# Kernel optimization log

Hardware: AMD Instinct MI355X
Metric: run time of the kernel (lower is better)

## Reference

```python
import jax, jax.numpy as jnp
import numpy as np

N_NODES = 100000
N_EDGES = 1600000
IN_DIM, HID_DIM, OUT_DIM = 128, 64, 1


def setup_inputs() -> dict:
    key = jax.random.key(0)
    ks = jax.random.split(key, 8)
    x = jax.random.normal(ks[0], (N_NODES, IN_DIM), dtype=jnp.float32)
    edge_index = jax.random.randint(ks[1], (2, N_EDGES), 0, N_NODES, dtype=jnp.int64)
    # Glorot-ish scaled weights
    W1 = jax.random.normal(ks[2], (IN_DIM, HID_DIM), dtype=jnp.float32) / np.sqrt(IN_DIM)
    b1 = jnp.zeros((HID_DIM,), dtype=jnp.float32)
    W2 = jax.random.normal(ks[3], (HID_DIM, HID_DIM), dtype=jnp.float32) / np.sqrt(HID_DIM)
    b2 = jnp.zeros((HID_DIM,), dtype=jnp.float32)
    W3 = jax.random.normal(ks[4], (HID_DIM, OUT_DIM), dtype=jnp.float32) / np.sqrt(HID_DIM)
    b3 = jnp.zeros((OUT_DIM,), dtype=jnp.float32)
    return {"x": x, "edge_index": edge_index, "W1": W1, "b1": b1,
            "W2": W2, "b2": b2, "W3": W3, "b3": b3}


def _gcn_norm(edge_index, num_nodes):
    # PyG gcn_norm with add_self_loops=True, edge_weight=1:
    # deg[i] = 1 (self loop) + #incoming edges at i (dst = edge_index[1])
    dst = edge_index[1]
    deg = jnp.ones((num_nodes,), dtype=jnp.float32).at[dst].add(1.0)
    dis = jnp.where(deg > 0, 1.0 / jnp.sqrt(deg), 0.0)  # deg_inv_sqrt
    return dis


def _gcn_conv(x, W, b, src, dst, dis):
    h = x @ W                                   # [N, F_out] transform first (PyG order)
    norm = dis[src] * dis[dst]                  # [E]
    msg = h[src] * norm[:, None]                # gather + scale, [E, F_out]
    out = jnp.zeros_like(h).at[dst].add(msg)    # scatter-add aggregation
    out = out + h * (dis * dis)[:, None]        # self-loop contribution
    return out + b


def reference(x, edge_index, W1, b1, W2, b2, W3, b3):
    src, dst = edge_index[0], edge_index[1]
    dis = _gcn_norm(edge_index, x.shape[0])
    h = jax.nn.relu(_gcn_conv(x, W1, b1, src, dst, dis))   # dropout = identity (eval)
    h = jax.nn.relu(_gcn_conv(h, W2, b2, src, dst, dis))
    return _gcn_conv(h, W3, b3, src, dst, dis)
```

## Files before the change

kernel.cpp:

```cpp
#include <hip/hip_runtime.h>

#define IN_DIM 128
#define HID 64
#define MAXC 400
#define MAXB 256
#define EPB 8192
#define DPT 1024
#define G1CAP 6144

static __device__ __forceinline__ unsigned short f2bf(float f) {
    unsigned u = __float_as_uint(f);
    u += 0x7FFF + ((u >> 16) & 1);
    return (unsigned short)(u >> 16);
}

typedef short bf16x8 __attribute__((ext_vector_type(8)));
typedef float f32x4 __attribute__((ext_vector_type(4)));

__global__ __launch_bounds__(256) void k_hist2(const int* __restrict__ dst,
                                               int* __restrict__ hmat, int E, int NC) {
    __shared__ int h[MAXC];
    int tid = threadIdx.x, blk = blockIdx.x;
    for (int i = tid; i < NC; i += 256) h[i] = 0;
    __syncthreads();
    int e0 = blk * EPB, e1 = min(e0 + EPB, E);
    for (int e = e0 + tid; e < e1; e += 256) atomicAdd(&h[dst[e] >> 8], 1);
    __syncthreads();
    for (int i = tid; i < NC; i += 256) hmat[blk * MAXC + i] = h[i];
}

__global__ __launch_bounds__(256) void k_bktscan(int* __restrict__ hmat,
                                                 int* __restrict__ bktTotal,
                                                 int NBLK, int NC) {
    __shared__ int tmp[256];
    int cb = blockIdx.x;
    int t = threadIdx.x;
    int v = (t < NBLK) ? hmat[t * MAXC + cb] : 0;
    tmp[t] = v;
    __syncthreads();
    for (int off = 1; off < 256; off <<= 1) {
        int a = (t >= off) ? tmp[t - off] : 0;
        __syncthreads();
        tmp[t] += a;
        __syncthreads();
    }
    if (t < NBLK) hmat[t * MAXC + cb] = tmp[t] - v;
    if (t == 255) bktTotal[cb] = tmp[255];
}

__global__ __launch_bounds__(512) void k_cscan(const int* __restrict__ bktTotal,
                                               int* __restrict__ coarseStart,
                                               int* __restrict__ rowStart,
                                               int NC, int N, int E) {
    __shared__ int tmp[512];
    int t = threadIdx.x;
    int v = (t < NC) ? bktTotal[t] : 0;
    tmp[t] = v;
    __syncthreads();
    for (int off = 1; off < 512; off <<= 1) {
        int a = (t >= off) ? tmp[t - off] : 0;
        __syncthreads();
        tmp[t] += a;
        __syncthreads();
    }
    int excl = tmp[t] - v;
    if (t < NC) coarseStart[t] = excl;
    if (t == NC - 1) coarseStart[NC] = excl + v;
    if (t == 0) rowStart[N] = E;
}

__global__ __launch_bounds__(256) void k_part1(const int* __restrict__ src,
                                               const int* __restrict__ dst,
                                               const int* __restrict__ hmat,
                                               const int* __restrict__ coarseStart,
                                               int* __restrict__ tmp1,
                                               int E, int NC) {
    __shared__ int bcnt[MAXC];
    __shared__ int bbase[MAXC];
    int tid = threadIdx.x, blk = blockIdx.x;
    for (int i = tid; i < NC; i += 256) {
        bcnt[i] = 0;
        bbase[i] = coarseStart[i] + hmat[blk * MAXC + i];
    }
    __syncthreads();
    int e0 = blk * EPB, e1 = min(e0 + EPB, E);
    for (int e = e0 + tid; e < e1; e += 256) {
        int s = src[e], d = dst[e];
        int cb = d >> 8;
        int slot = bbase[cb] + atomicAdd(&bcnt[cb], 1);
        tmp1[slot] = s | ((d & 255) << 17);
    }
}

__global__ __launch_bounds__(DPT) void k_degplace(const int* __restrict__ tmp1,
                                                  const int* __restrict__ coarseStart,
                                                  float* __restrict__ dis,
                                                  int* __restrict__ rowStart,
                                                  int* __restrict__ esrc, int N) {
    __shared__ int hist[256];
    __shared__ int scn[256];
    __shared__ int cur[256];
    int tid = threadIdx.x;
    int cb = blockIdx.x;
    int node0 = cb << 8;
    const int r0 = coarseStart[cb], r1 = coarseStart[cb + 1];
    if (tid < 256) hist[tid] = 0;
    __syncthreads();
    for (int i = r0 + tid; i < r1; i += DPT)
        atomicAdd(&hist[((unsigned)tmp1[i]) >> 17], 1);
    __syncthreads();
    int v = 0;
    if (tid < 256) { v = hist[tid]; scn[tid] = v; }
    __syncthreads();
    for (int off = 1; off < 256; off <<= 1) {
        int a = 0;
        if (tid < 256 && tid >= off) a = scn[tid - off];
        __syncthreads();
        if (tid < 256) scn[tid] += a;
        __syncthreads();
    }
    if (tid < 256) {
        int myStart = r0 + scn[tid] - v;
        cur[tid] = myStart;
        int node = node0 + tid;
        if (node < N) {
            dis[node] = rsqrtf((float)v + 1.0f);
            rowStart[node] = myStart;
        }
    }
    __syncthreads();
    for (int i = r0 + tid; i < r1; i += DPT) {
        int pk = tmp1[i];
        int dl = ((unsigned)pk) >> 17;
        int pos = atomicAdd(&cur[dl], 1);
        esrc[pos] = (pk & 0x1FFFF) << 7;
    }
}

template <int K, typename T>
__global__ __launch_bounds__(256) void k_mmx(const T* __restrict__ X,
                                             const float* __restrict__ W,
                                             const float* __restrict__ dis,
                                             unsigned short* __restrict__ Hbs, int N) {
    constexpr int WP = K + 8;
    __shared__ unsigned short Wt[64 * WP];
    const int tid = threadIdx.x;
    for (int i = tid; i < K * 64; i += 256) {
        int k = i >> 6, n = i & 63;
        Wt[n * WP + k] = f2bf(W[i]);
    }
    __syncthreads();
    const int lane = tid & 63;
    const int m16 = lane & 15;
    const int quad = lane >> 4;
    const int rowBase = blockIdx.x * 64 + (tid >> 6) * 16;
    const int rowc = min(rowBase + m16, N - 1);

    f32x4 acc0 = {0.f, 0.f, 0.f, 0.f};
    f32x4 acc1 = acc0, acc2 = acc0, acc3 = acc0;
    const T* xrow = X + (size_t)rowc * K;
#pragma unroll
    for (int k0 = 0; k0 < K; k0 += 32) {
        bf16x8 af;
        if constexpr (sizeof(T) == 4) {
            const float* xp = (const float*)xrow + k0 + quad * 8;
            float4 xa = *(const float4*)xp;
            float4 xb = *(const float4*)(xp + 4);
            af[0] = (short)f2bf(xa.x); af[1] = (short)f2bf(xa.y);
            af[2] = (short)f2bf(xa.z); af[3] = (short)f2bf(xa.w);
            af[4] = (short)f2bf(xb.x); af[5] = (short)f2bf(xb.y);
            af[6] = (short)f2bf(xb.z); af[7] = (short)f2bf(xb.w);
        } else {
            af = *(const bf16x8*)((const unsigned short*)xrow + k0 + quad * 8);
        }
        const unsigned short* wp = &Wt[m16 * WP + k0 + quad * 8];
        bf16x8 b0 = *(const bf16x8*)(wp);
        bf16x8 b1 = *(const bf16x8*)(wp + 16 * WP);
        bf16x8 b2 = *(const bf16x8*)(wp + 32 * WP);
        bf16x8 b3 = *(const bf16x8*)(wp + 48 * WP);
        acc0 = __builtin_amdgcn_mfma_f32_16x16x32_bf16(af, b0, acc0, 0, 0, 0);
        acc1 = __builtin_amdgcn_mfma_f32_16x16x32_bf16(af, b1, acc1, 0, 0, 0);
        acc2 = __builtin_amdgcn_mfma_f32_16x16x32_bf16(af, b2, acc2, 0, 0, 0);
        acc3 = __builtin_amdgcn_mfma_f32_16x16x32_bf16(af, b3, acc3, 0, 0, 0);
    }
#pragma unroll
    for (int reg = 0; reg < 4; ++reg) {
        int r = rowBase + quad * 4 + reg;
        if (r < N) {
            float dsc = dis[r];
            unsigned short* hp = Hbs + (size_t)r * 64 + m16;
            hp[0]  = f2bf(acc0[reg] * dsc);
            hp[16] = f2bf(acc1[reg] * dsc);
            hp[32] = f2bf(acc2[reg] * dsc);
            hp[48] = f2bf(acc3[reg] * dsc);
        }
    }
}


#define ACCADD(A, D)                                                           \
    {                                                                          \
        A.x += __uint_as_float((D).x << 16);                                   \
        A.y += __uint_as_float((D).x & 0xFFFF0000u);                           \
        A.z += __uint_as_float((D).y << 16);                                   \
        A.w += __uint_as_float((D).y & 0xFFFF0000u);                           \
    }

#define GNODE4(ACC, RA, RB)                                                    \
    {                                                                          \
        int j0 = max(RA - base, 0);                                            \
        int j1 = min(RB - base, cnt);                                          \
        int j = j0;                                                            \
        for (; j + 16 <= j1; j += 16) {                                        \
            unsigned o0 = __shfl(eoff, j + sub, 64);                           \
            unsigned o1 = __shfl(eoff, j + 4 + sub, 64);                       \
            unsigned o2 = __shfl(eoff, j + 8 + sub, 64);                       \
            unsigned o3 = __shfl(eoff, j + 12 + sub, 64);                      \
            uint2 q0 = *(const uint2*)(hb + o0);                               \
            uint2 q1 = *(const uint2*)(hb + o1);                               \
            uint2 q2 = *(const uint2*)(hb + o2);                               \
            uint2 q3 = *(const uint2*)(hb + o3);                               \
            ACCADD(ACC, q0) ACCADD(ACC, q1) ACCADD(ACC, q2) ACCADD(ACC, q3)    \
        }                                                                      \
        if (j + 8 <= j1) {                                                     \
            unsigned o0 = __shfl(eoff, j + sub, 64);                           \
            unsigned o1 = __shfl(eoff, j + 4 + sub, 64);                       \
            uint2 q0 = *(const uint2*)(hb + o0);                               \
            uint2 q1 = *(const uint2*)(hb + o1);                               \
            ACCADD(ACC, q0) ACCADD(ACC, q1)                                    \
            j += 8;                                                            \
        }                                                                      \
        if (j + 4 <= j1) {                                                     \
            unsigned o0 = __shfl(eoff, j + sub, 64);                           \
            uint2 q0 = *(const uint2*)(hb + o0);                               \
            ACCADD(ACC, q0)                                                    \
            j += 4;                                                            \
        }                                                                      \
        if (j < j1) {                                                          \
            int idx = j + sub;                                                 \
            bool vld = idx < j1;                                               \
            unsigned o0 = __shfl(eoff, vld ? idx : j0, 64);                    \
            uint2 q0 = *(const uint2*)(hb + o0);                               \
            if (!vld) { q0.x = 0u; q0.y = 0u; }                                \
            ACCADD(ACC, q0)                                                    \
        }                                                                      \
    }

#define REDX(A)                                                                \
    {                                                                          \
        A.x += __shfl_xor(A.x, 16, 64); A.y += __shfl_xor(A.y, 16, 64);        \
        A.z += __shfl_xor(A.z, 16, 64); A.w += __shfl_xor(A.w, 16, 64);        \
        A.x += __shfl_xor(A.x, 32, 64); A.y += __shfl_xor(A.y, 32, 64);        \
        A.z += __shfl_xor(A.z, 32, 64); A.w += __shfl_xor(A.w, 32, 64);        \
    }

template <int MODE>
__global__ __launch_bounds__(256) void k_gather64(const unsigned short* __restrict__ Hbs,
                                                  const int* __restrict__ esrc,
                                                  const int* __restrict__ rowStart,
                                                  const float* __restrict__ dis,
                                                  const float* __restrict__ b,
                                                  unsigned short* __restrict__ outB,
                                                  const float* __restrict__ W3,
                                                  const float* __restrict__ b3,
                                                  float* __restrict__ colS,
                                                  float* __restrict__ outF,
                                                  int N) {
    int lane = threadIdx.x & 63;
    int c = lane & 15;
    int sub = lane >> 4;
    int wave = (blockIdx.x * 256 + threadIdx.x) >> 6;
    int g0 = wave * 4;
    if (g0 >= N) return;
    const char* hb = (const char*)Hbs + c * 8;

    int rb = rowStart[min(g0 + lane, N)];
    int R0 = __shfl(rb, 0, 64), R1 = __shfl(rb, 1, 64);
    int R2 = __shfl(rb, 2, 64), R3 = __shfl(rb, 3, 64);
    int R4 = __shfl(rb, 4, 64);

    float4 a0 = {0.f, 0.f, 0.f, 0.f}, a1 = a0, a2 = a0, a3 = a0;
    {
        int nself = min(g0 + sub, N - 1);
        uint2 sd = *(const uint2*)(hb + ((size_t)nself << 7));
        float4 sf;
        sf.x = __uint_as_float(sd.x << 16);
        sf.y = __uint_as_float(sd.x & 0xFFFF0000u);
        sf.z = __uint_as_float(sd.y << 16);
        sf.w = __uint_as_float(sd.y & 0xFFFF0000u);
        if (sub == 0) a0 = sf;
        else if (sub == 1) a1 = sf;
        else if (sub == 2) a2 = sf;
        else a3 = sf;
    }

    for (int base = R0; base < R4; base += 64) {
        int cnt = min(64, R4 - base);
        unsigned eoff = (lane < cnt) ? (unsigned)esrc[base + lane] : 0u;
        GNODE4(a0, R0, R1)
        GNODE4(a1, R1, R2)
        GNODE4(a2, R2, R3)
        GNODE4(a3, R3, R4)
    }

    REDX(a0) REDX(a1) REDX(a2) REDX(a3)

    float4 a = a0;
    if (sub == 1) a = a1;
    if (sub == 2) a = a2;
    if (sub == 3) a = a3;
    int node = g0 + sub;
    float ds = dis[min(node, N - 1)];
    float4 bl = ((const float4*)b)[c];
    float4 v;
    v.x = fmaxf(a.x * ds + bl.x, 0.f);
    v.y = fmaxf(a.y * ds + bl.y, 0.f);
    v.z = fmaxf(a.z * ds + bl.z, 0.f);
    v.w = fmaxf(a.w * ds + bl.w, 0.f);

    if (MODE == 1) {
        uint2 pv;
        pv.x = (unsigned)f2bf(v.x) | ((unsigned)f2bf(v.y) << 16);
        pv.y = (unsigned)f2bf(v.z) | ((unsigned)f2bf(v.w) << 16);
        if (node < N) ((uint2*)outB)[(size_t)node * 16 + c] = pv;
    } else {
        float4 w3 = ((const float4*)W3)[c];
        float t = v.x * w3.x + v.y * w3.y + v.z * w3.z + v.w * w3.w;
        t += __shfl_xor(t, 1, 64);
        t += __shfl_xor(t, 2, 64);
        t += __shfl_xor(t, 4, 64);
        t += __shfl_xor(t, 8, 64);
        if (c == 0 && node < N) {
            colS[node] = t * ds;
            outF[node] = t * ds * ds + b3[0];
        }
    }
}

__global__ __launch_bounds__(256) void k_gather1(const float* __restrict__ colS,
                                                 const int* __restrict__ esrc,
                                                 const int* __restrict__ rowStart,
                                                 const float* __restrict__ dis,
                                                 float* __restrict__ out, int N) {
    __shared__ float ls[G1CAP];
    int tid = threadIdx.x;
    int n0 = blockIdx.x * 256;
    int nEnd = min(n0 + 256, N);
    int r0 = rowStart[n0];
    int r1 = rowStart[nEnd];
    int cnt = r1 - r0;
    if (cnt <= G1CAP) {
        for (int i = tid; i < cnt; i += 256)
            ls[i] = colS[((unsigned)esrc[r0 + i]) >> 7];
        __syncthreads();
        int n = n0 + tid;
        if (n < N) {
            int a = rowStart[n] - r0, bnd = rowStart[n + 1] - r0;
            float acc = 0.0f;
            for (int e = a; e < bnd; ++e) acc += ls[e];
            out[n] += acc * dis[n];
        }
    } else {
        int n = n0 + tid;
        if (n < N) {
            int a = rowStart[n], bnd = rowStart[n + 1];
            float acc = 0.0f;
            for (int e = a; e < bnd; ++e) acc += colS[((unsigned)esrc[e]) >> 7];
            out[n] += acc * dis[n];
        }
    }
}

extern "C" void kernel_launch(void* const* d_in, const int* in_sizes, int n_in,
                              void* d_out, int out_size, void* d_ws, size_t ws_size,
                              hipStream_t stream) {
    const float* x  = (const float*)d_in[0];
    const int*   ei = (const int*)d_in[1];
    const float* W1 = (const float*)d_in[2];
    const float* b1 = (const float*)d_in[3];
    const float* W2 = (const float*)d_in[4];
    const float* b2 = (const float*)d_in[5];
    const float* W3 = (const float*)d_in[6];
    const float* b3 = (const float*)d_in[7];
    float* out = (float*)d_out;

    const int N = in_sizes[0] / IN_DIM;
    const int E = in_sizes[1] / 2;
    const int* src = ei;
    const int* dst = ei + E;
    const int NC = (N + 255) >> 8;
    const int NBLK = (E + EPB - 1) / EPB;

    char* w = (char*)d_ws;
    auto alloc = [&](size_t bytes) {
        char* p = w;
        w += (bytes + 1023) & ~(size_t)1023;
        return p;
    };
    float*          dis        = (float*)alloc((size_t)N * 4);
    unsigned short* Hbs        = (unsigned short*)alloc((size_t)N * 64 * 2);
    unsigned short* Hb1        = (unsigned short*)alloc((size_t)N * 64 * 2);
    float*          colS       = (float*)alloc((size_t)N * 4);
    int*            rowStart   = (int*)alloc((size_t)(N + 1) * 4);
    int*            bktTotal   = (int*)alloc((size_t)MAXC * 4);
    int*            coarseStart= (int*)alloc((size_t)(MAXC + 1) * 4);
    int*            hmat       = (int*)alloc((size_t)MAXB * MAXC * 4);
    int*            esrc       = (int*)alloc((size_t)E * 4);
    int*            tmp1       = (int*)alloc((size_t)E * 4);

    const int NB_N  = (N + 255) / 256;
    const int NB_MX = (N + 63) / 64;
    const int NB_G4 = ((N + 3) / 4 * 64 + 255) / 256;

    k_hist2<<<NBLK, 256, 0, stream>>>(dst, hmat, E, NC);
    k_bktscan<<<NC, 256, 0, stream>>>(hmat, bktTotal, NBLK, NC);
    k_cscan<<<1, 512, 0, stream>>>(bktTotal, coarseStart, rowStart, NC, N, E);
    k_part1<<<NBLK, 256, 0, stream>>>(src, dst, hmat, coarseStart, tmp1, E, NC);
    k_degplace<<<NC, DPT, 0, stream>>>(tmp1, coarseStart, dis, rowStart, esrc, N);

    k_mmx<IN_DIM, float><<<NB_MX, 256, 0, stream>>>(x, W1, dis, Hbs, N);
    k_gather64<1><<<NB_G4, 256, 0, stream>>>(Hbs, esrc, rowStart, dis, b1,
                                             Hb1, nullptr, nullptr, nullptr, nullptr, N);

    k_mmx<HID, unsigned short><<<NB_MX, 256, 0, stream>>>(Hb1, W2, dis, Hbs, N);
    k_gather64<2><<<NB_G4, 256, 0, stream>>>(Hbs, esrc, rowStart, dis, b2,
                                             nullptr, W3, b3, colS, out, N);

    k_gather1<<<NB_N, 256, 0, stream>>>(colS, esrc, rowStart, dis, out, N);
}
```

Baseline: 242.3 us.

## Assign one node per quarter-wave in GCN gather and retune CSR build sizes

```diff
diff --git a/kernel.cpp b/kernel.cpp
--- a/kernel.cpp
+++ b/kernel.cpp
@@ -3,9 +3,9 @@
 #define IN_DIM 128
 #define HID 64
 #define MAXC 400
-#define MAXB 256
-#define EPB 8192
-#define DPT 1024
+#define MAXB 512
+#define EPB 4096
+#define DPT 512
 #define G1CAP 6144
 
 static __device__ __forceinline__ unsigned short f2bf(float f) {
@@ -29,23 +29,23 @@
     for (int i = tid; i < NC; i += 256) hmat[blk * MAXC + i] = h[i];
 }
 
-__global__ __launch_bounds__(256) void k_bktscan(int* __restrict__ hmat,
+__global__ __launch_bounds__(512) void k_bktscan(int* __restrict__ hmat,
                                                  int* __restrict__ bktTotal,
                                                  int NBLK, int NC) {
-    __shared__ int tmp[256];
+    __shared__ int tmp[512];
     int cb = blockIdx.x;
     int t = threadIdx.x;
     int v = (t < NBLK) ? hmat[t * MAXC + cb] : 0;
     tmp[t] = v;
     __syncthreads();
-    for (int off = 1; off < 256; off <<= 1) {
+    for (int off = 1; off < 512; off <<= 1) {
         int a = (t >= off) ? tmp[t - off] : 0;
         __syncthreads();
         tmp[t] += a;
         __syncthreads();
     }
     if (t < NBLK) hmat[t * MAXC + cb] = tmp[t] - v;
-    if (t == 255) bktTotal[cb] = tmp[255];
+    if (t == 511) bktTotal[cb] = tmp[511];
 }
 
 __global__ __launch_bounds__(512) void k_cscan(const int* __restrict__ bktTotal,
@@ -198,61 +198,10 @@
 }
 
 
-#define ACCADD(A, D)                                                           \
-    {                                                                          \
-        A.x += __uint_as_float((D).x << 16);                                   \
-        A.y += __uint_as_float((D).x & 0xFFFF0000u);                           \
-        A.z += __uint_as_float((D).y << 16);                                   \
-        A.w += __uint_as_float((D).y & 0xFFFF0000u);                           \
-    }
-
-#define GNODE4(ACC, RA, RB)                                                    \
-    {                                                                          \
-        int j0 = max(RA - base, 0);                                            \
-        int j1 = min(RB - base, cnt);                                          \
-        int j = j0;                                                            \
-        for (; j + 16 <= j1; j += 16) {                                        \
-            unsigned o0 = __shfl(eoff, j + sub, 64);                           \
-            unsigned o1 = __shfl(eoff, j + 4 + sub, 64);                       \
-            unsigned o2 = __shfl(eoff, j + 8 + sub, 64);                       \
-            unsigned o3 = __shfl(eoff, j + 12 + sub, 64);                      \
-            uint2 q0 = *(const uint2*)(hb + o0);                               \
-            uint2 q1 = *(const uint2*)(hb + o1);                               \
-            uint2 q2 = *(const uint2*)(hb + o2);                               \
-            uint2 q3 = *(const uint2*)(hb + o3);                               \
-            ACCADD(ACC, q0) ACCADD(ACC, q1) ACCADD(ACC, q2) ACCADD(ACC, q3)    \
-        }                                                                      \
-        if (j + 8 <= j1) {                                                     \
-            unsigned o0 = __shfl(eoff, j + sub, 64);                           \
-            unsigned o1 = __shfl(eoff, j + 4 + sub, 64);                       \
-            uint2 q0 = *(const uint2*)(hb + o0);                               \
-            uint2 q1 = *(const uint2*)(hb + o1);                               \
-            ACCADD(ACC, q0) ACCADD(ACC, q1)                                    \
-            j += 8;                                                            \
-        }                                                                      \
-        if (j + 4 <= j1) {                                                     \
-            unsigned o0 = __shfl(eoff, j + sub, 64);                           \
-            uint2 q0 = *(const uint2*)(hb + o0);                               \
-            ACCADD(ACC, q0)                                                    \
-            j += 4;                                                            \
-        }                                                                      \
-        if (j < j1) {                                                          \
-            int idx = j + sub;                                                 \
-            bool vld = idx < j1;                                               \
-            unsigned o0 = __shfl(eoff, vld ? idx : j0, 64);                    \
-            uint2 q0 = *(const uint2*)(hb + o0);                               \
-            if (!vld) { q0.x = 0u; q0.y = 0u; }                                \
-            ACCADD(ACC, q0)                                                    \
-        }                                                                      \
-    }
-
-#define REDX(A)                                                                \
-    {                                                                          \
-        A.x += __shfl_xor(A.x, 16, 64); A.y += __shfl_xor(A.y, 16, 64);        \
-        A.z += __shfl_xor(A.z, 16, 64); A.w += __shfl_xor(A.w, 16, 64);        \
-        A.x += __shfl_xor(A.x, 32, 64); A.y += __shfl_xor(A.y, 32, 64);        \
-        A.z += __shfl_xor(A.z, 32, 64); A.w += __shfl_xor(A.w, 32, 64);        \
-    }
+#define BLO(d) __uint_as_float((d) << 16)
+#define BHI(d) __uint_as_float((d) & 0xFFFF0000u)
+#define ACC2(A, Q) { A.x += BLO((Q).x); A.y += BHI((Q).x);                     \
+                     A.z += BLO((Q).y); A.w += BHI((Q).y); }
 
 template <int MODE>
 __global__ __launch_bounds__(256) void k_gather64(const unsigned short* __restrict__ Hbs,
@@ -269,48 +218,78 @@
     int lane = threadIdx.x & 63;
     int c = lane & 15;
     int sub = lane >> 4;
+    int qb = sub << 4;
     int wave = (blockIdx.x * 256 + threadIdx.x) >> 6;
     int g0 = wave * 4;
     if (g0 >= N) return;
     const char* hb = (const char*)Hbs + c * 8;
 
     int rb = rowStart[min(g0 + lane, N)];
-    int R0 = __shfl(rb, 0, 64), R1 = __shfl(rb, 1, 64);
-    int R2 = __shfl(rb, 2, 64), R3 = __shfl(rb, 3, 64);
-    int R4 = __shfl(rb, 4, 64);
-
-    float4 a0 = {0.f, 0.f, 0.f, 0.f}, a1 = a0, a2 = a0, a3 = a0;
+    int Rq  = __shfl(rb, sub, 64);
+    int Rq1 = __shfl(rb, sub + 1, 64);
+    int n = g0 + sub;
+    int nc = min(n, N - 1);
+
+    float4 a;
     {
-        int nself = min(g0 + sub, N - 1);
-        uint2 sd = *(const uint2*)(hb + ((size_t)nself << 7));
-        float4 sf;
-        sf.x = __uint_as_float(sd.x << 16);
-        sf.y = __uint_as_float(sd.x & 0xFFFF0000u);
-        sf.z = __uint_as_float(sd.y << 16);
-        sf.w = __uint_as_float(sd.y & 0xFFFF0000u);
-        if (sub == 0) a0 = sf;
-        else if (sub == 1) a1 = sf;
-        else if (sub == 2) a2 = sf;
-        else a3 = sf;
-    }
-
-    for (int base = R0; base < R4; base += 64) {
-        int cnt = min(64, R4 - base);
-        unsigned eoff = (lane < cnt) ? (unsigned)esrc[base + lane] : 0u;
-        GNODE4(a0, R0, R1)
-        GNODE4(a1, R1, R2)
-        GNODE4(a2, R2, R3)
-        GNODE4(a3, R3, R4)
-    }
-
-    REDX(a0) REDX(a1) REDX(a2) REDX(a3)
-
-    float4 a = a0;
-    if (sub == 1) a = a1;
-    if (sub == 2) a = a2;
-    if (sub == 3) a = a3;
-    int node = g0 + sub;
-    float ds = dis[min(node, N - 1)];
+        uint2 sd = *(const uint2*)(hb + ((size_t)nc << 7));
+        a.x = BLO(sd.x); a.y = BHI(sd.x); a.z = BLO(sd.y); a.w = BHI(sd.y);
+    }
+
+    unsigned eoff = (Rq + c < Rq1) ? (unsigned)esrc[Rq + c] : 0u;
+    for (int bb = Rq; bb < Rq1; bb += 16) {
+        int cnt = min(16, Rq1 - bb);
+        unsigned eoffN = (bb + 16 + c < Rq1) ? (unsigned)esrc[bb + 16 + c] : 0u;
+
+        int j = 0;
+        for (; j + 8 <= cnt; j += 8) {
+            unsigned o0 = __shfl(eoff, qb + j + 0, 64);
+            unsigned o1 = __shfl(eoff, qb + j + 1, 64);
+            unsigned o2 = __shfl(eoff, qb + j + 2, 64);
+            unsigned o3 = __shfl(eoff, qb + j + 3, 64);
+            unsigned o4 = __shfl(eoff, qb + j + 4, 64);
+            unsigned o5 = __shfl(eoff, qb + j + 5, 64);
+            unsigned o6 = __shfl(eoff, qb + j + 6, 64);
+            unsigned o7 = __shfl(eoff, qb + j + 7, 64);
+            uint2 q0 = *(const uint2*)(hb + o0);
+            uint2 q1 = *(const uint2*)(hb + o1);
+            uint2 q2 = *(const uint2*)(hb + o2);
+            uint2 q3 = *(const uint2*)(hb + o3);
+            uint2 q4 = *(const uint2*)(hb + o4);
+            uint2 q5 = *(const uint2*)(hb + o5);
+            uint2 q6 = *(const uint2*)(hb + o6);
+            uint2 q7 = *(const uint2*)(hb + o7);
+            ACC2(a, q0) ACC2(a, q1) ACC2(a, q2) ACC2(a, q3)
+            ACC2(a, q4) ACC2(a, q5) ACC2(a, q6) ACC2(a, q7)
+        }
+        if (j + 4 <= cnt) {
+            unsigned o0 = __shfl(eoff, qb + j + 0, 64);
+            unsigned o1 = __shfl(eoff, qb + j + 1, 64);
+            unsigned o2 = __shfl(eoff, qb + j + 2, 64);
+            unsigned o3 = __shfl(eoff, qb + j + 3, 64);
+            uint2 q0 = *(const uint2*)(hb + o0);
+            uint2 q1 = *(const uint2*)(hb + o1);
+            uint2 q2 = *(const uint2*)(hb + o2);
+            uint2 q3 = *(const uint2*)(hb + o3);
+            ACC2(a, q0) ACC2(a, q1) ACC2(a, q2) ACC2(a, q3)
+            j += 4;
+        }
+        if (j < cnt) {
+            bool v1 = j + 1 < cnt, v2 = j + 2 < cnt;
+            unsigned o0 = __shfl(eoff, qb + j, 64);
+            unsigned o1 = __shfl(eoff, v1 ? qb + j + 1 : qb + j, 64);
+            unsigned o2 = __shfl(eoff, v2 ? qb + j + 2 : qb + j, 64);
+            uint2 q0 = *(const uint2*)(hb + o0);
+            uint2 q1 = *(const uint2*)(hb + o1);
+            uint2 q2 = *(const uint2*)(hb + o2);
+            if (!v1) { q1.x = 0u; q1.y = 0u; }
+            if (!v2) { q2.x = 0u; q2.y = 0u; }
+            ACC2(a, q0) ACC2(a, q1) ACC2(a, q2)
+        }
+        eoff = eoffN;
+    }
+
+    float ds = dis[nc];
     float4 bl = ((const float4*)b)[c];
     float4 v;
     v.x = fmaxf(a.x * ds + bl.x, 0.f);
@@ -322,7 +301,7 @@
         uint2 pv;
         pv.x = (unsigned)f2bf(v.x) | ((unsigned)f2bf(v.y) << 16);
         pv.y = (unsigned)f2bf(v.z) | ((unsigned)f2bf(v.w) << 16);
-        if (node < N) ((uint2*)outB)[(size_t)node * 16 + c] = pv;
+        if (n < N) ((uint2*)outB)[(size_t)n * 16 + c] = pv;
     } else {
         float4 w3 = ((const float4*)W3)[c];
         float t = v.x * w3.x + v.y * w3.y + v.z * w3.z + v.w * w3.w;
@@ -330,9 +309,9 @@
         t += __shfl_xor(t, 2, 64);
         t += __shfl_xor(t, 4, 64);
         t += __shfl_xor(t, 8, 64);
-        if (c == 0 && node < N) {
-            colS[node] = t * ds;
-            outF[node] = t * ds * ds + b3[0];
+        if (c == 0 && n < N) {
+            colS[n] = t * ds;
+            outF[n] = t * ds * ds + b3[0];
         }
     }
 }
@@ -413,7 +392,7 @@
     const int NB_G4 = ((N + 3) / 4 * 64 + 255) / 256;
 
     k_hist2<<<NBLK, 256, 0, stream>>>(dst, hmat, E, NC);
-    k_bktscan<<<NC, 256, 0, stream>>>(hmat, bktTotal, NBLK, NC);
+    k_bktscan<<<NC, 512, 0, stream>>>(hmat, bktTotal, NBLK, NC);
     k_cscan<<<1, 512, 0, stream>>>(bktTotal, coarseStart, rowStart, NC, N, E);
     k_part1<<<NBLK, 256, 0, stream>>>(src, dst, hmat, coarseStart, tmp1, E, NC);
     k_degplace<<<NC, DPT, 0, stream>>>(tmp1, coarseStart, dis, rowStart, esrc, N);
```

Result: faster. 233.3 us (-3.7%).
